# Kernel optimization log

Measured on AMD Instinct MI355X. Metric: run time of the kernel, lower is better.

Reference implementation:

```python
import jax, jax.numpy as jnp
import numpy as np

NUM_GRAPHS = 128

def _gcn_conv(x, W, b, src, dst, deg_inv_sqrt, n_nodes):
    # PyG GCNConv: h = X W; out[dst] += d^-1/2[src] * d^-1/2[dst] * h[src]; out += b
    h = x @ W
    norm = deg_inv_sqrt[src] * deg_inv_sqrt[dst]  # [E]
    msg = h[src] * norm[:, None]                  # [E, C]
    out = jax.ops.segment_sum(msg, dst, num_segments=n_nodes)
    return out + b


def setup_inputs() -> dict:
    key = jax.random.key(0)
    k1, k2, k3, k4, k5 = jax.random.split(key, 5)
    n_nodes, n_edges, c_in, c_hid = 50000, 800000, 256, 256
    x = jax.random.normal(k1, (n_nodes, c_in), dtype=jnp.float32)
    edge_index = jax.random.randint(k2, (2, n_edges), 0, n_nodes, dtype=jnp.int64)
    batch = jnp.sort(jax.random.randint(k3, (n_nodes,), 0, NUM_GRAPHS, dtype=jnp.int64))
    s1 = 1.0 / np.sqrt(c_in)
    s2 = 1.0 / np.sqrt(c_hid)
    W1 = jax.random.uniform(k4, (c_in, c_hid), jnp.float32, -s1, s1)
    b1 = jnp.zeros((c_hid,), jnp.float32)
    W2 = jax.random.uniform(k5, (c_hid, c_hid), jnp.float32, -s2, s2)
    b2 = jnp.zeros((c_hid,), jnp.float32)
    return {"x": x, "edge_index": edge_index, "batch": batch,
            "W1": W1, "b1": b1, "W2": W2, "b2": b2}


def reference(x, edge_index, batch, W1, b1, W2, b2):
    n_nodes = x.shape[0]
    # add self-loops (GCNConv default add_self_loops=True)
    loops = jnp.arange(n_nodes, dtype=edge_index.dtype)
    src = jnp.concatenate([edge_index[0], loops])
    dst = jnp.concatenate([edge_index[1], loops])
    deg = jax.ops.segment_sum(jnp.ones_like(dst, dtype=x.dtype), dst, num_segments=n_nodes)
    deg_inv_sqrt = jnp.where(deg > 0, jax.lax.rsqrt(deg), 0.0)

    h = jax.nn.relu(_gcn_conv(x, W1, b1, src, dst, deg_inv_sqrt, n_nodes))
    # dropout p=0.2 is identity in eval mode
    h = jax.nn.relu(_gcn_conv(h, W2, b2, src, dst, deg_inv_sqrt, n_nodes))

    # global mean pool over graph ids
    sums = jax.ops.segment_sum(h, batch, num_segments=NUM_GRAPHS)
    cnts = jax.ops.segment_sum(jnp.ones((n_nodes,), h.dtype), batch, num_segments=NUM_GRAPHS)
    return sums / jnp.maximum(cnts, 1.0)[:, None]
```

## Files before the change

kernel.cpp:

```cpp
#include <hip/hip_runtime.h>

#define NCH 256
#define NS  16

typedef short short8 __attribute__((ext_vector_type(8)));
typedef float f32x4  __attribute__((ext_vector_type(4)));

__device__ __forceinline__ float b2f(unsigned short u) {
    union { unsigned int i; float f; } x; x.i = ((unsigned int)u) << 16; return x.f;
}
__device__ __forceinline__ unsigned short f2b(float f) {
    unsigned int u = __float_as_uint(f);
    unsigned int r = (u + 0x7FFFu + ((u >> 16) & 1u)) >> 16;
    return (unsigned short)r;
}

#define GLOAD_LDS16(gptr, lptr) \
    __builtin_amdgcn_global_load_lds((const __attribute__((address_space(1))) void*)(gptr), \
                                     (__attribute__((address_space(3))) void*)(lptr), 16, 0, 0)

__global__ __launch_bounds__(256) void k_pre(const int* __restrict__ dst, int E,
                                             int* __restrict__ deg, int nh,
                                             unsigned shmul,
                                             const float* __restrict__ W1,
                                             const float* __restrict__ W2,
                                             unsigned short* __restrict__ Wt1,
                                             unsigned short* __restrict__ Wt2) {
    int b = blockIdx.x;
    if (b < nh) {
        const int shard  = b & 7;
        const int nchunk = nh >> 3;
        const int chunk  = b >> 3;
        const int per = (E + nchunk - 1) / nchunk;
        const int e0 = chunk * per;
        const int e1 = min(e0 + per, E);
        for (int e = e0 + threadIdx.x; e < e1; e += 256) {
            int d = dst[e];
            if ((int)__umulhi((unsigned)d, shmul) == shard)
                atomicAdd(&deg[d], 1);
        }
    } else {
        int k = (b - nh) & 255;
        const float* W = ((b - nh) >> 8) ? W2 : W1;
        unsigned short* Wt = ((b - nh) >> 8) ? Wt2 : Wt1;
        int n = threadIdx.x;
        Wt[(size_t)n * 256 + k] = f2b(W[(size_t)k * 256 + n]);
    }
}

__global__ __launch_bounds__(256) void k_scan_blk(const int* __restrict__ deg,
                                                  int* __restrict__ part,
                                                  int* __restrict__ bsum, int N) {
    __shared__ int sm[256];
    int t = threadIdx.x;
    int base = blockIdx.x * 1024 + t * 4;
    int v[4]; int s = 0;
#pragma unroll
    for (int j = 0; j < 4; ++j) {
        int i = base + j;
        int d = (i < N) ? deg[i] : 0;
        v[j] = d; s += d;
    }
    sm[t] = s; __syncthreads();
#pragma unroll
    for (int off = 1; off < 256; off <<= 1) {
        int u = (t >= off) ? sm[t - off] : 0;
        __syncthreads();
        sm[t] += u;
        __syncthreads();
    }
    int excl = sm[t] - s;
#pragma unroll
    for (int j = 0; j < 4; ++j) {
        int i = base + j;
        if (i < N) part[i] = excl;
        excl += v[j];
    }
    if (t == 255) bsum[blockIdx.x] = sm[255];
}

__global__ void k_scan_top(int* __restrict__ bsum, int nb, int* __restrict__ rowptr_end) {
    int t = threadIdx.x;
    int orig = (t < nb) ? bsum[t] : 0;
    int v = orig;
#pragma unroll
    for (int off = 1; off < 64; off <<= 1) {
        int u = __shfl_up(v, off, 64);
        if (t >= off) v += u;
    }
    if (t < nb) bsum[t] = v - orig;
    if (t == 63) *rowptr_end = v;
}

__global__ __launch_bounds__(256) void k_finalize(const int* __restrict__ deg,
                                                  int* __restrict__ row_ptr,
                                                  const int* __restrict__ boff,
                                                  int* __restrict__ cursor,
                                                  float* __restrict__ dinv, int N) {
    int i = blockIdx.x * 256 + threadIdx.x;
    if (i < N) {
        int rp = row_ptr[i] + boff[i >> 10];
        row_ptr[i] = rp;
        cursor[i]  = rp;
        dinv[i] = rsqrtf((float)(deg[i] + 1));
    }
}

__global__ __launch_bounds__(256) void k_scatter_sh(const int* __restrict__ src,
                                                    const int* __restrict__ dst, int E,
                                                    int* __restrict__ cursor,
                                                    const float* __restrict__ dinv,
                                                    int2* __restrict__ cw,
                                                    unsigned shmul) {
    const int shard  = blockIdx.x & 7;
    const int nchunk = gridDim.x >> 3;
    const int chunk  = blockIdx.x >> 3;
    const int per = (E + nchunk - 1) / nchunk;
    const int e0 = chunk * per;
    const int e1 = min(e0 + per, E);
    for (int e = e0 + threadIdx.x; e < e1; e += 256) {
        int d = dst[e];
        int s = (int)__umulhi((unsigned)d, shmul);
        if (s == shard) {
            int sv = src[e];
            int pos = atomicAdd(&cursor[d], 1);
            cw[pos] = make_int2(sv, __float_as_int(dinv[sv]));
        }
    }
}


__device__ __forceinline__ void gemm_compute_store(const unsigned short* As,
                                                   const short8 bfr[2][8],
                                                   unsigned short* __restrict__ C,
                                                   int M, int t, int w, int lr, int ku) {
    f32x4 acc[2][2];
#pragma unroll
    for (int rf = 0; rf < 2; ++rf)
#pragma unroll
        for (int nf = 0; nf < 2; ++nf) acc[rf][nf] = (f32x4){0.f, 0.f, 0.f, 0.f};

#pragma unroll
    for (int ks = 0; ks < 8; ++ks) {
#pragma unroll
        for (int rf = 0; rf < 2; ++rf) {
            int row = rf * 16 + lr;
            int uu  = (ks * 4 + ku) ^ (row & 7);
            short8 af = *(const short8*)&As[row * 256 + uu * 8];
            acc[rf][0] = __builtin_amdgcn_mfma_f32_16x16x32_bf16(bfr[0][ks], af,
                                                                 acc[rf][0], 0, 0, 0);
            acc[rf][1] = __builtin_amdgcn_mfma_f32_16x16x32_bf16(bfr[1][ks], af,
                                                                 acc[rf][1], 0, 0, 0);
        }
    }

#pragma unroll
    for (int rf = 0; rf < 2; ++rf) {
        int row = t * 32 + rf * 16 + lr;
        if (row < M) {
            unsigned short* pc = C + (size_t)row * NCH + w * 32 + ku * 4;
#pragma unroll
            for (int nf = 0; nf < 2; ++nf) {
                unsigned short us[4];
                us[0] = f2b(acc[rf][nf][0]); us[1] = f2b(acc[rf][nf][1]);
                us[2] = f2b(acc[rf][nf][2]); us[3] = f2b(acc[rf][nf][3]);
                *(int2*)(pc + nf * 16) = *(const int2*)us;
            }
        }
    }
}

__device__ __forceinline__ void load_bfr(const unsigned short* __restrict__ Bt,
                                         short8 bfr[2][8], int w, int lr, int ku) {
    const unsigned short* pb = Bt + (size_t)(w * 32 + lr) * NCH + ku * 8;
#pragma unroll
    for (int nf = 0; nf < 2; ++nf)
#pragma unroll
        for (int ks = 0; ks < 8; ++ks)
            bfr[nf][ks] = *(const short8*)(pb + nf * 16 * NCH + ks * 32);
}

__global__ __launch_bounds__(512, 4) void k_gemm2(const unsigned short* __restrict__ A,
                                                  const unsigned short* __restrict__ Bt,
                                                  unsigned short* __restrict__ C, int M) {
    __shared__ unsigned short As[32 * 256];
    const int tid  = threadIdx.x;
    const int w    = tid >> 6;
    const int lane = tid & 63;
    const int lr   = lane & 15;
    const int ku   = lane >> 4;
    const int t    = blockIdx.x;

    short8 bfr[2][8];
    load_bfr(Bt, bfr, w, lr, ku);

#pragma unroll
    for (int j = 0; j < 2; ++j) {
        int gu = w * 128 + j * 64 + lane;
        int r  = gu >> 5;
        int u  = gu & 31;
        int grow = t * 32 + r; if (grow >= M) grow = M - 1;
        const unsigned short* gp = A + (size_t)grow * NCH + ((u ^ (r & 7)) << 3);
        GLOAD_LDS16(gp, As + (size_t)(w * 128 + j * 64) * 8);
    }
    __syncthreads();

    gemm_compute_store(As, bfr, C, M, t, w, lr, ku);
}

__global__ __launch_bounds__(512, 4) void k_gemm1(const float* __restrict__ A,
                                                  const unsigned short* __restrict__ Bt,
                                                  unsigned short* __restrict__ C, int M) {
    __shared__ unsigned short As[32 * 256];
    const int tid  = threadIdx.x;
    const int w    = tid >> 6;
    const int lane = tid & 63;
    const int lr   = lane & 15;
    const int ku   = lane >> 4;
    const int t    = blockIdx.x;

    short8 bfr[2][8];
    load_bfr(Bt, bfr, w, lr, ku);

#pragma unroll
    for (int j = 0; j < 2; ++j) {
        int unit = tid + j * 512;
        int r = unit >> 5;
        int u = unit & 31;
        int grow = t * 32 + r; if (grow >= M) grow = M - 1;
        const float* pa = A + (size_t)grow * NCH + u * 8;
        float4 f0 = *(const float4*)pa;
        float4 f1 = *(const float4*)(pa + 4);
        unsigned short us[8];
        us[0] = f2b(f0.x); us[1] = f2b(f0.y); us[2] = f2b(f0.z); us[3] = f2b(f0.w);
        us[4] = f2b(f1.x); us[5] = f2b(f1.y); us[6] = f2b(f1.z); us[7] = f2b(f1.w);
        *(int4*)&As[r * 256 + ((u ^ (r & 7)) << 3)] = *(const int4*)us;
    }
    __syncthreads();

    gemm_compute_store(As, bfr, C, M, t, w, lr, ku);
}

__global__ __launch_bounds__(256) void k_agg_w(const unsigned short* __restrict__ h,
                                               const float* __restrict__ dinv,
                                               const int* __restrict__ row_ptr,
                                               const int2* __restrict__ cw,
                                               const float* __restrict__ bias,
                                               unsigned short* __restrict__ out, int M) {
    int v = blockIdx.x * 4 + (threadIdx.x >> 6);
    if (v >= M) return;
    const int lane = threadIdx.x & 63;
    const int half = lane >> 5;
    const int cb   = (lane & 31) << 3;

    float acc[8] = {};
    float dv = dinv[v];

    short8 rs = {};
    if (half == 0) rs = *(const short8*)&h[(size_t)v * NCH + cb];

    int beg = row_ptr[v], end = row_ptr[v + 1];
    int i0 = beg + half * 2;

    short8 r0 = {}, r1 = {};
    float  w0 = 0.f, w1 = 0.f;
    bool b0 = i0 < end, b1 = i0 + 1 < end;
    if (b0) {
        int2 e = cw[i0];
        r0 = *(const short8*)&h[(size_t)e.x * NCH + cb];
        w0 = __int_as_float(e.y);
    }
    if (b1) {
        int2 e = cw[i0 + 1];
        r1 = *(const short8*)&h[(size_t)e.x * NCH + cb];
        w1 = __int_as_float(e.y);
    }

    while (b0) {
        int in = i0 + 4;
        bool n0 = in < end, n1 = in + 1 < end;
        short8 s0 = {}, s1 = {};
        float  x0 = 0.f, x1 = 0.f;
        if (n0) {
            int2 e = cw[in];
            s0 = *(const short8*)&h[(size_t)e.x * NCH + cb];
            x0 = __int_as_float(e.y);
        }
        if (n1) {
            int2 e = cw[in + 1];
            s1 = *(const short8*)&h[(size_t)e.x * NCH + cb];
            x1 = __int_as_float(e.y);
        }
#pragma unroll
        for (int i = 0; i < 8; ++i) acc[i] += w0 * b2f((unsigned short)r0[i]);
#pragma unroll
        for (int i = 0; i < 8; ++i) acc[i] += w1 * b2f((unsigned short)r1[i]);
        r0 = s0; r1 = s1; w0 = x0; w1 = x1; b0 = n0; b1 = n1; i0 = in;
    }

    if (half == 0) {
#pragma unroll
        for (int i = 0; i < 8; ++i) acc[i] += dv * b2f((unsigned short)rs[i]);
    }

#pragma unroll
    for (int i = 0; i < 8; ++i) acc[i] += __shfl_xor(acc[i], 32, 64);

    if (half == 0) {
        f32x4 bl = *(const f32x4*)&bias[cb];
        f32x4 bh = *(const f32x4*)&bias[cb + 4];
        unsigned short us[8];
#pragma unroll
        for (int i = 0; i < 8; ++i) {
            float b = (i < 4) ? bl[i] : bh[i - 4];
            us[i] = f2b(fmaxf(dv * acc[i] + b, 0.0f));
        }
        *(int4*)&out[(size_t)v * NCH + cb] = *(const int4*)us;
    }
}

__device__ __forceinline__ int lower_bound_i(const int* a, int n, int key) {
    int lo = 0, hi = n;
    while (lo < hi) {
        int mid = (lo + hi) >> 1;
        if (a[mid] < key) lo = mid + 1; else hi = mid;
    }
    return lo;
}

__global__ __launch_bounds__(64) void k_pool_a(const unsigned short* __restrict__ a,
                                               const int* __restrict__ batch,
                                               float* __restrict__ partial, int N) {
    int g = blockIdx.x, s = blockIdx.y;
    const int lane = threadIdx.x;
    const int half = lane >> 5;
    const int cb   = (lane & 31) << 3;

    int lo = lower_bound_i(batch, N, g);
    int hi = lower_bound_i(batch, N, g + 1);
    int cnt = hi - lo;
    int len = (cnt + NS - 1) / NS;
    int rlo = lo + s * len;
    int rhi = min(rlo + len, hi);

    float acc[8] = {};
    for (int r = rlo + half; r < rhi; r += 2) {
        short8 hv = *(const short8*)&a[(size_t)r * NCH + cb];
#pragma unroll
        for (int i = 0; i < 8; ++i) acc[i] += b2f((unsigned short)hv[i]);
    }
#pragma unroll
    for (int i = 0; i < 8; ++i) acc[i] += __shfl_xor(acc[i], 32, 64);

    if (half == 0) {
        float* p = partial + ((size_t)g * NS + s) * NCH + cb;
        *(f32x4*)p       = (f32x4){acc[0], acc[1], acc[2], acc[3]};
        *(f32x4*)(p + 4) = (f32x4){acc[4], acc[5], acc[6], acc[7]};
    }
}

__global__ __launch_bounds__(256) void k_pool_b(const float* __restrict__ partial,
                                                const int* __restrict__ batch,
                                                float* __restrict__ out, int N) {
    int g = blockIdx.x, ch = threadIdx.x;
    int lo = lower_bound_i(batch, N, g);
    int hi = lower_bound_i(batch, N, g + 1);
    float s = 0.0f;
#pragma unroll
    for (int k = 0; k < NS; ++k)
        s += partial[((size_t)g * NS + k) * NCH + ch];
    out[(size_t)g * NCH + ch] = s / (float)max(hi - lo, 1);
}

extern "C" void kernel_launch(void* const* d_in, const int* in_sizes, int n_in,
                              void* d_out, int out_size, void* d_ws, size_t ws_size,
                              hipStream_t stream) {
    const float* x     = (const float*)d_in[0];
    const int*   ei    = (const int*)d_in[1];
    const int*   batch = (const int*)d_in[2];
    const float* W1    = (const float*)d_in[3];
    const float* b1    = (const float*)d_in[4];
    const float* W2    = (const float*)d_in[5];
    const float* b2    = (const float*)d_in[6];
    float* out = (float*)d_out;

    const int M = in_sizes[0] / NCH;
    const int E = in_sizes[1] / 2;
    const int* src = ei;
    const int* dst = ei + E;

    char* w = (char*)d_ws;
    auto alloc = [&](size_t bytes) -> void* {
        void* p = (void*)w;
        w += (bytes + 255) & ~(size_t)255;
        return p;
    };
    int*   deg     = (int*)alloc((size_t)M * 4);
    float* dinv    = (float*)alloc((size_t)M * 4);
    int*   row_ptr = (int*)alloc((size_t)(M + 1) * 4);
    int*   cursor  = (int*)alloc((size_t)M * 4);
    int*   bsum    = (int*)alloc(64 * 4);
    int2*  cw      = (int2*)alloc((size_t)E * 8);
    unsigned short* bufP = (unsigned short*)alloc((size_t)M * NCH * 2);
    unsigned short* bufQ = (unsigned short*)alloc((size_t)M * NCH * 2);
    unsigned short* Wt1  = (unsigned short*)alloc((size_t)NCH * NCH * 2);
    unsigned short* Wt2  = (unsigned short*)alloc((size_t)NCH * NCH * 2);
    float* partial = (float*)alloc((size_t)128 * NS * NCH * 4);

    const int nb = (M + 1023) / 1024;
    const unsigned shmul = (unsigned)(((8ull << 32) + M - 1) / (unsigned long long)M);
    const int tiles = (M + 31) / 32;
    const int nh = 2048;

    hipMemsetAsync(deg, 0, (size_t)M * 4, stream);
    k_pre<<<nh + 512, 256, 0, stream>>>(dst, E, deg, nh, shmul, W1, W2, Wt1, Wt2);
    k_scan_blk<<<nb, 256, 0, stream>>>(deg, row_ptr, bsum, M);
    k_scan_top<<<1, 64, 0, stream>>>(bsum, nb, row_ptr + M);
    k_finalize<<<(M + 255) / 256, 256, 0, stream>>>(deg, row_ptr, bsum, cursor, dinv, M);
    k_scatter_sh<<<4096, 256, 0, stream>>>(src, dst, E, cursor, dinv, cw, shmul);

    const int agrid = (M + 3) / 4;

    k_gemm1<<<tiles, 512, 0, stream>>>(x, Wt1, bufP, M);
    k_agg_w<<<agrid, 256, 0, stream>>>(bufP, dinv, row_ptr, cw, b1, bufQ, M);
    k_gemm2<<<tiles, 512, 0, stream>>>(bufQ, Wt2, bufP, M);
    k_agg_w<<<agrid, 256, 0, stream>>>(bufP, dinv, row_ptr, cw, b2, bufQ, M);
    k_pool_a<<<dim3(128, NS), 64, 0, stream>>>(bufQ, batch, partial, M);
    k_pool_b<<<128, 256, 0, stream>>>(partial, batch, out, M);
}
```

Before: 306.5 us.

## Make GEMM kernels persistent with double-buffered LDS prefetch of next tile

Both GEMM kernels now run as a fixed grid of 512 persistent blocks that loop over 32-row tiles. While the current tile is computed, the next tile's A rows are prefetched into a second LDS buffer, via async global-to-LDS loads in gemm2 and register loads plus bf16 conversion in gemm1. This keeps the weight fragments in registers across tiles, so they are loaded once per block rather than once per tile, and hides global load latency. In exchange LDS use per block doubles, which may lower occupancy, and the fixed grid may balance work less evenly across CUs.

```diff
diff --git a/kernel.cpp b/kernel.cpp
--- a/kernel.cpp
+++ b/kernel.cpp
@@ -129,6 +129,15 @@
     }
 }
 
+__device__ __forceinline__ void load_bfr(const unsigned short* __restrict__ Bt,
+                                         short8 bfr[2][8], int w, int lr, int ku) {
+    const unsigned short* pb = Bt + (size_t)(w * 32 + lr) * NCH + ku * 8;
+#pragma unroll
+    for (int nf = 0; nf < 2; ++nf)
+#pragma unroll
+        for (int ks = 0; ks < 8; ++ks)
+            bfr[nf][ks] = *(const short8*)(pb + nf * 16 * NCH + ks * 32);
+}
 
 __device__ __forceinline__ void gemm_compute_store(const unsigned short* As,
                                                    const short8 bfr[2][8],
@@ -170,75 +179,112 @@
     }
 }
 
-__device__ __forceinline__ void load_bfr(const unsigned short* __restrict__ Bt,
-                                         short8 bfr[2][8], int w, int lr, int ku) {
-    const unsigned short* pb = Bt + (size_t)(w * 32 + lr) * NCH + ku * 8;
-#pragma unroll
-    for (int nf = 0; nf < 2; ++nf)
-#pragma unroll
-        for (int ks = 0; ks < 8; ++ks)
-            bfr[nf][ks] = *(const short8*)(pb + nf * 16 * NCH + ks * 32);
-}
-
 __global__ __launch_bounds__(512, 4) void k_gemm2(const unsigned short* __restrict__ A,
                                                   const unsigned short* __restrict__ Bt,
-                                                  unsigned short* __restrict__ C, int M) {
-    __shared__ unsigned short As[32 * 256];
+                                                  unsigned short* __restrict__ C,
+                                                  int M, int tiles) {
+    __shared__ unsigned short As[2][32 * 256];
     const int tid  = threadIdx.x;
     const int w    = tid >> 6;
     const int lane = tid & 63;
     const int lr   = lane & 15;
     const int ku   = lane >> 4;
-    const int t    = blockIdx.x;
 
     short8 bfr[2][8];
     load_bfr(Bt, bfr, w, lr, ku);
 
-#pragma unroll
-    for (int j = 0; j < 2; ++j) {
-        int gu = w * 128 + j * 64 + lane;
-        int r  = gu >> 5;
-        int u  = gu & 31;
-        int grow = t * 32 + r; if (grow >= M) grow = M - 1;
-        const unsigned short* gp = A + (size_t)grow * NCH + ((u ^ (r & 7)) << 3);
-        GLOAD_LDS16(gp, As + (size_t)(w * 128 + j * 64) * 8);
-    }
+    const int gu0 = w * 128 + lane;
+
+#define STAGE2(tt, buf) do {                                                  \
+        _Pragma("unroll")                                                     \
+        for (int j = 0; j < 2; ++j) {                                         \
+            int gu = gu0 + j * 64;                                            \
+            int r  = gu >> 5;                                                 \
+            int u  = gu & 31;                                                 \
+            int grow = (tt) * 32 + r; if (grow >= M) grow = M - 1;            \
+            const unsigned short* gp = A + (size_t)grow * NCH +               \
+                                       ((u ^ (r & 7)) << 3);                  \
+            GLOAD_LDS16(gp, (buf) + (size_t)(w * 128 + j * 64) * 8);          \
+        }                                                                     \
+    } while (0)
+
+    int t = blockIdx.x;
+    int cur = 0;
+    if (t < tiles) STAGE2(t, As[0]);
     __syncthreads();
 
-    gemm_compute_store(As, bfr, C, M, t, w, lr, ku);
+    for (; t < tiles; t += gridDim.x) {
+        int tn = t + gridDim.x;
+        if (tn < tiles) STAGE2(tn, As[cur ^ 1]);
+        gemm_compute_store(As[cur], bfr, C, M, t, w, lr, ku);
+        __syncthreads();
+        cur ^= 1;
+    }
+#undef STAGE2
 }
 
 __global__ __launch_bounds__(512, 4) void k_gemm1(const float* __restrict__ A,
                                                   const unsigned short* __restrict__ Bt,
-                                                  unsigned short* __restrict__ C, int M) {
-    __shared__ unsigned short As[32 * 256];
+                                                  unsigned short* __restrict__ C,
+                                                  int M, int tiles) {
+    __shared__ unsigned short As[2][32 * 256];
     const int tid  = threadIdx.x;
     const int w    = tid >> 6;
     const int lane = tid & 63;
     const int lr   = lane & 15;
     const int ku   = lane >> 4;
-    const int t    = blockIdx.x;
 
     short8 bfr[2][8];
     load_bfr(Bt, bfr, w, lr, ku);
 
-#pragma unroll
-    for (int j = 0; j < 2; ++j) {
-        int unit = tid + j * 512;
-        int r = unit >> 5;
-        int u = unit & 31;
-        int grow = t * 32 + r; if (grow >= M) grow = M - 1;
-        const float* pa = A + (size_t)grow * NCH + u * 8;
-        float4 f0 = *(const float4*)pa;
-        float4 f1 = *(const float4*)(pa + 4);
+    const int r0_ = tid >> 5,          u0_ = tid & 31;
+    const int r1_ = (tid + 512) >> 5,  u1_ = (tid + 512) & 31;
+
+    int t = blockIdx.x;
+    int cur = 0;
+    if (t < tiles) {
+        int g0 = t * 32 + r0_; if (g0 >= M) g0 = M - 1;
+        int g1 = t * 32 + r1_; if (g1 >= M) g1 = M - 1;
+        const float4* pa0 = (const float4*)(A + (size_t)g0 * NCH + u0_ * 8);
+        const float4* pa1 = (const float4*)(A + (size_t)g1 * NCH + u1_ * 8);
+        float4 a0 = pa0[0], a1 = pa0[1];
+        float4 b0 = pa1[0], b1 = pa1[1];
         unsigned short us[8];
-        us[0] = f2b(f0.x); us[1] = f2b(f0.y); us[2] = f2b(f0.z); us[3] = f2b(f0.w);
-        us[4] = f2b(f1.x); us[5] = f2b(f1.y); us[6] = f2b(f1.z); us[7] = f2b(f1.w);
-        *(int4*)&As[r * 256 + ((u ^ (r & 7)) << 3)] = *(const int4*)us;
+        us[0]=f2b(a0.x); us[1]=f2b(a0.y); us[2]=f2b(a0.z); us[3]=f2b(a0.w);
+        us[4]=f2b(a1.x); us[5]=f2b(a1.y); us[6]=f2b(a1.z); us[7]=f2b(a1.w);
+        *(int4*)&As[0][r0_ * 256 + ((u0_ ^ (r0_ & 7)) << 3)] = *(const int4*)us;
+        us[0]=f2b(b0.x); us[1]=f2b(b0.y); us[2]=f2b(b0.z); us[3]=f2b(b0.w);
+        us[4]=f2b(b1.x); us[5]=f2b(b1.y); us[6]=f2b(b1.z); us[7]=f2b(b1.w);
+        *(int4*)&As[0][r1_ * 256 + ((u1_ ^ (r1_ & 7)) << 3)] = *(const int4*)us;
     }
     __syncthreads();
 
-    gemm_compute_store(As, bfr, C, M, t, w, lr, ku);
+    for (; t < tiles; t += gridDim.x) {
+        int tn = t + gridDim.x;
+        float4 a0, a1, b0, b1;
+        if (tn < tiles) {
+            int g0 = tn * 32 + r0_; if (g0 >= M) g0 = M - 1;
+            int g1 = tn * 32 + r1_; if (g1 >= M) g1 = M - 1;
+            const float4* pa0 = (const float4*)(A + (size_t)g0 * NCH + u0_ * 8);
+            const float4* pa1 = (const float4*)(A + (size_t)g1 * NCH + u1_ * 8);
+            a0 = pa0[0]; a1 = pa0[1];
+            b0 = pa1[0]; b1 = pa1[1];
+        }
+
+        gemm_compute_store(As[cur], bfr, C, M, t, w, lr, ku);
+
+        if (tn < tiles) {
+            unsigned short us[8];
+            us[0]=f2b(a0.x); us[1]=f2b(a0.y); us[2]=f2b(a0.z); us[3]=f2b(a0.w);
+            us[4]=f2b(a1.x); us[5]=f2b(a1.y); us[6]=f2b(a1.z); us[7]=f2b(a1.w);
+            *(int4*)&As[cur ^ 1][r0_ * 256 + ((u0_ ^ (r0_ & 7)) << 3)] = *(const int4*)us;
+            us[0]=f2b(b0.x); us[1]=f2b(b0.y); us[2]=f2b(b0.z); us[3]=f2b(b0.w);
+            us[4]=f2b(b1.x); us[5]=f2b(b1.y); us[6]=f2b(b1.z); us[7]=f2b(b1.w);
+            *(int4*)&As[cur ^ 1][r1_ * 256 + ((u1_ ^ (r1_ & 7)) << 3)] = *(const int4*)us;
+        }
+        __syncthreads();
+        cur ^= 1;
+    }
 }
 
 __global__ __launch_bounds__(256) void k_agg_w(const unsigned short* __restrict__ h,
@@ -412,18 +458,19 @@
     const int tiles = (M + 31) / 32;
     const int nh = 2048;
 
-    hipMemsetAsync(deg, 0, (size_t)M * 4, stream);
+    (void)hipMemsetAsync(deg, 0, (size_t)M * 4, stream);
     k_pre<<<nh + 512, 256, 0, stream>>>(dst, E, deg, nh, shmul, W1, W2, Wt1, Wt2);
     k_scan_blk<<<nb, 256, 0, stream>>>(deg, row_ptr, bsum, M);
     k_scan_top<<<1, 64, 0, stream>>>(bsum, nb, row_ptr + M);
     k_finalize<<<(M + 255) / 256, 256, 0, stream>>>(deg, row_ptr, bsum, cursor, dinv, M);
     k_scatter_sh<<<4096, 256, 0, stream>>>(src, dst, E, cursor, dinv, cw, shmul);
 
+    const int ggrid = 512;
     const int agrid = (M + 3) / 4;
 
-    k_gemm1<<<tiles, 512, 0, stream>>>(x, Wt1, bufP, M);
+    k_gemm1<<<ggrid, 512, 0, stream>>>(x, Wt1, bufP, M, tiles);
     k_agg_w<<<agrid, 256, 0, stream>>>(bufP, dinv, row_ptr, cw, b1, bufQ, M);
-    k_gemm2<<<tiles, 512, 0, stream>>>(bufQ, Wt2, bufP, M);
+    k_gemm2<<<ggrid, 512, 0, stream>>>(bufQ, Wt2, bufP, M, tiles);
     k_agg_w<<<agrid, 256, 0, stream>>>(bufP, dinv, row_ptr, cw, b2, bufQ, M);
     k_pool_a<<<dim3(128, NS), 64, 0, stream>>>(bufQ, batch, partial, M);
     k_pool_b<<<128, 256, 0, stream>>>(partial, batch, out, M);
```

After: 276.5 us. 1.11x faster.
